# Kernel tuning notes

Measured on AMD Instinct MI355X. Metric: run time of the kernel, lower is better.

The kernel has to match this reference:

```python
import jax, jax.numpy as jnp
import numpy as np

N = 100_000
E = 1_000_000
D = 64
NORM_FACTOR = 100.0
LN_EPS = 1e-5


def setup_inputs() -> dict:
    key = jax.random.key(0)
    ks = jax.random.split(key, 8)
    h = jax.random.normal(ks[0], (N, D), dtype=jnp.float32)
    distances = jax.random.uniform(ks[1], (E, 1), dtype=jnp.float32)
    edges = jax.random.randint(ks[2], (2, E), 0, N, dtype=jnp.int64)
    node_mask = jnp.ones((N, 1), dtype=jnp.float32)
    edge_mask = jnp.ones((E, 1), dtype=jnp.float32)
    s = 1.0 / np.sqrt(D)
    W_lin = jax.random.normal(ks[3], (D, D), dtype=jnp.float32) * s
    b_lin = jnp.zeros((D,), dtype=jnp.float32)
    att_W1 = jax.random.normal(ks[4], (D, 2 * D + 1), dtype=jnp.float32) * (1.0 / np.sqrt(2 * D + 1))
    att_b1 = jnp.zeros((D,), dtype=jnp.float32)
    att_W2 = jax.random.normal(ks[5], (1, D), dtype=jnp.float32) * s
    att_b2 = jnp.zeros((1,), dtype=jnp.float32)
    ln_g = jnp.ones((D,), dtype=jnp.float32)
    ln_b = jnp.zeros((D,), dtype=jnp.float32)
    return {"h": h, "distances": distances, "edges": edges, "node_mask": node_mask,
            "edge_mask": edge_mask, "W_lin": W_lin, "b_lin": b_lin,
            "att_W1": att_W1, "att_b1": att_b1, "att_W2": att_W2, "att_b2": att_b2,
            "ln_g": ln_g, "ln_b": ln_b}


def reference(h, distances, edges, node_mask, edge_mask, W_lin, b_lin,
              att_W1, att_b1, att_W2, att_b2, ln_g, ln_b):
    # Linear projection: [N, D]
    x = h @ W_lin.T + b_lin
    row, col = edges[0], edges[1]
    x_row = x[row]          # [E, D]
    x_col = x[col]          # [E, D]
    # DenseAtt: MLP(concat(x_row, x_col, dist)) -> sigmoid -> * edge_mask
    cat = jnp.concatenate([x_row, x_col, distances], axis=1)  # [E, 2D+1]
    hdn = jax.nn.silu(cat @ att_W1.T + att_b1)                # [E, D]
    att = jax.nn.sigmoid(hdn @ att_W2.T + att_b2) * edge_mask # [E, 1]
    # Attention-weighted scatter-sum aggregation into row segments
    agg = x_col * att
    out = jax.ops.segment_sum(agg, row, num_segments=x.shape[0]) / NORM_FACTOR
    out = out + x           # residual
    # LayerNorm + activation
    mu = jnp.mean(out, axis=-1, keepdims=True)
    var = jnp.mean(jnp.square(out - mu), axis=-1, keepdims=True)
    y = (out - mu) * jax.lax.rsqrt(var + LN_EPS) * ln_g + ln_b
    return jax.nn.silu(y)
```

## Files before the change

### kernel.cpp

```cpp
#include <hip/hip_runtime.h>
#include <hip/hip_bf16.h>

#define N_NODES 100000
#define N_EDGES 1000000
#define DIM 64
#define NORM_INV 0.01f
#define LN_EPS 1e-5f
#define N_TILES 6250
#define PROJ_BLOCKS 1563
#define N_BUCKETS 782
#define HISTB 489
#define L2E 1.4426950408889634f
#define LN2 0.6931471805599453f
#define CAP 2560
#define RPT 5

typedef __attribute__((ext_vector_type(8))) short short8;
typedef __attribute__((ext_vector_type(4))) float f32x4;

__device__ __forceinline__ unsigned short f2bf(float f) {
    union { float f; unsigned u; } x; x.f = f;
    unsigned r = x.u + 0x7FFFu + ((x.u >> 16) & 1u);
    return (unsigned short)(r >> 16);
}
__device__ __forceinline__ float bf2f(unsigned short s) {
    union { unsigned u; float f; } x; x.u = ((unsigned)s) << 16; return x.f;
}

__global__ __launch_bounds__(256) void prep_frags(
    const float* __restrict__ W, const float* __restrict__ att_W1,
    const float* __restrict__ att_b1, const float* __restrict__ att_W2,
    short8* __restrict__ whi, short8* __restrict__ wlo,
    short8* __restrict__ wa, short8* __restrict__ wb,
    float4* __restrict__ tab) {
    const int l = threadIdx.x & 63;
    const int nt = threadIdx.x >> 6;
    const int c = l & 15, q = l >> 4;
    const int n = nt * 16 + c;
#pragma unroll
    for (int ks = 0; ks < 2; ++ks) {
        const int k0 = ks * 32 + q * 8;
        short8 hi8, lo8, a8, b8;
#pragma unroll
        for (int jj = 0; jj < 8; ++jj) {
            float w = W[n * 64 + k0 + jj];
            unsigned short hh = f2bf(w);
            hi8[jj] = (short)hh;
            lo8[jj] = (short)f2bf(w - bf2f(hh));
            a8[jj] = (short)f2bf(att_W1[n * 129 + k0 + jj]);
            b8[jj] = (short)f2bf(att_W1[n * 129 + 64 + k0 + jj]);
        }
        const int idx = (nt * 2 + ks) * 64 + l;
        whi[idx] = hi8; wlo[idx] = lo8; wa[idx] = a8; wb[idx] = b8;
    }
    if (threadIdx.x < 64) {
        const int f = threadIdx.x;
        tab[f] = make_float4(att_W2[f] * LN2, att_W1[f * 129 + 128] * L2E,
                             att_b1[f] * L2E, 0.f);
    }
}

__global__ __launch_bounds__(256) void proj_hist(
    const float* __restrict__ h, const float* __restrict__ bl,
    const short8* __restrict__ whi, const short8* __restrict__ wlo,
    const short8* __restrict__ wa, const short8* __restrict__ wb,
    const int* __restrict__ edges, int* __restrict__ bucketCnt,
    unsigned short* __restrict__ xv, unsigned short* __restrict__ u_bf) {
    if (blockIdx.x >= PROJ_BLOCKS) {
        __shared__ int lh[N_BUCKETS];
        const int tid = threadIdx.x;
        for (int i = tid; i < N_BUCKETS; i += 256) lh[i] = 0;
        __syncthreads();
        const int e0 = (blockIdx.x - PROJ_BLOCKS) * 2048;
#pragma unroll
        for (int i = 0; i < 8; ++i) {
            const int e = e0 + tid * 8 + i;
            if (e < N_EDGES) atomicAdd(&lh[edges[e] >> 7], 1);
        }
        __syncthreads();
        for (int b = tid; b < N_BUCKETS; b += 256)
            if (lh[b]) atomicAdd(&bucketCnt[b], lh[b]);
        return;
    }
    __shared__ __align__(16) unsigned short lds[4][16 * 72];
    const int lane = threadIdx.x & 63;
    const int wv = threadIdx.x >> 6;
    const int c = lane & 15, q = lane >> 4;
    const int tile = blockIdx.x * 4 + wv;
    if (tile >= N_TILES) return;
    const int n0 = tile * 16;

    short8 Whi[4][2], Wlo[4][2], Wa[4][2], Wb[4][2];
    float bias[4];
#pragma unroll
    for (int nt = 0; nt < 4; ++nt) {
        bias[nt] = bl[nt * 16 + c];
#pragma unroll
        for (int ks = 0; ks < 2; ++ks) {
            const int idx = (nt * 2 + ks) * 64 + lane;
            Whi[nt][ks] = whi[idx]; Wlo[nt][ks] = wlo[idx];
            Wa[nt][ks] = wa[idx];   Wb[nt][ks] = wb[idx];
        }
    }

    short8 Ahi[2], Alo[2];
#pragma unroll
    for (int ks = 0; ks < 2; ++ks) {
        const float* hp = h + (size_t)(n0 + c) * 64 + ks * 32 + q * 8;
        f32x4 p0 = *(const f32x4*)hp;
        f32x4 p1 = *(const f32x4*)(hp + 4);
        short8 hi8, lo8;
#pragma unroll
        for (int jj = 0; jj < 4; ++jj) {
            unsigned short hh = f2bf(p0[jj]);
            hi8[jj] = (short)hh; lo8[jj] = (short)f2bf(p0[jj] - bf2f(hh));
            unsigned short h2 = f2bf(p1[jj]);
            hi8[4 + jj] = (short)h2; lo8[4 + jj] = (short)f2bf(p1[jj] - bf2f(h2));
        }
        Ahi[ks] = hi8; Alo[ks] = lo8;
    }

    f32x4 xacc[4] = {{0,0,0,0},{0,0,0,0},{0,0,0,0},{0,0,0,0}};
#pragma unroll
    for (int ks = 0; ks < 2; ++ks)
#pragma unroll
        for (int nt = 0; nt < 4; ++nt) {
            xacc[nt] = __builtin_amdgcn_mfma_f32_16x16x32_bf16(Ahi[ks], Whi[nt][ks], xacc[nt], 0, 0, 0);
            xacc[nt] = __builtin_amdgcn_mfma_f32_16x16x32_bf16(Ahi[ks], Wlo[nt][ks], xacc[nt], 0, 0, 0);
            xacc[nt] = __builtin_amdgcn_mfma_f32_16x16x32_bf16(Alo[ks], Whi[nt][ks], xacc[nt], 0, 0, 0);
        }

    unsigned short* lw = lds[wv];
#pragma unroll
    for (int r = 0; r < 4; ++r) {
        const int node = n0 + q * 4 + r;
        unsigned short xb[4];
#pragma unroll
        for (int nt = 0; nt < 4; ++nt) {
            unsigned short v16 = f2bf(xacc[nt][r] + bias[nt]);
            xb[nt] = v16;
            lw[(q * 4 + r) * 72 + nt * 16 + c] = v16;
        }
        uint2 pk;
        pk.x = (unsigned)xb[0] | ((unsigned)xb[1] << 16);
        pk.y = (unsigned)xb[2] | ((unsigned)xb[3] << 16);
        *(uint2*)(xv + (size_t)node * 128 + c * 8) = pk;
    }

    short8 Ax[2];
#pragma unroll
    for (int ks = 0; ks < 2; ++ks)
        Ax[ks] = *(const short8*)&lw[c * 72 + ks * 32 + q * 8];

    f32x4 uacc[4] = {{0,0,0,0},{0,0,0,0},{0,0,0,0},{0,0,0,0}};
    f32x4 vacc[4] = {{0,0,0,0},{0,0,0,0},{0,0,0,0},{0,0,0,0}};
#pragma unroll
    for (int ks = 0; ks < 2; ++ks)
#pragma unroll
        for (int nt = 0; nt < 4; ++nt) {
            uacc[nt] = __builtin_amdgcn_mfma_f32_16x16x32_bf16(Ax[ks], Wa[nt][ks], uacc[nt], 0, 0, 0);
            vacc[nt] = __builtin_amdgcn_mfma_f32_16x16x32_bf16(Ax[ks], Wb[nt][ks], vacc[nt], 0, 0, 0);
        }
#pragma unroll
    for (int r = 0; r < 4; ++r) {
        const int node = n0 + q * 4 + r;
        uint2 pu;
        pu.x = (unsigned)f2bf(uacc[0][r] * L2E) | ((unsigned)f2bf(uacc[1][r] * L2E) << 16);
        pu.y = (unsigned)f2bf(uacc[2][r] * L2E) | ((unsigned)f2bf(uacc[3][r] * L2E) << 16);
        *(uint2*)(u_bf + (size_t)node * 64 + c * 4) = pu;
        uint2 pk;
        pk.x = (unsigned)f2bf(vacc[0][r] * L2E) | ((unsigned)f2bf(vacc[1][r] * L2E) << 16);
        pk.y = (unsigned)f2bf(vacc[2][r] * L2E) | ((unsigned)f2bf(vacc[3][r] * L2E) << 16);
        *(uint2*)(xv + (size_t)node * 128 + c * 8 + 4) = pk;
    }
}

__global__ __launch_bounds__(1024) void scanA(
    const int* __restrict__ bucketCnt, int* __restrict__ baseA,
    int* __restrict__ cursA) {
    __shared__ int wsum[16];
    const int t = threadIdx.x, lane = t & 63, w = t >> 6;
    const int v = (t < N_BUCKETS) ? bucketCnt[t] : 0;
    int sc = v;
#pragma unroll
    for (int off = 1; off < 64; off <<= 1) {
        int u = __shfl_up(sc, off);
        if (lane >= off) sc += u;
    }
    if (lane == 63) wsum[w] = sc;
    __syncthreads();
    if (w == 0) {
        int x = (lane < 16) ? wsum[lane] : 0;
#pragma unroll
        for (int off = 1; off < 16; off <<= 1) {
            int u = __shfl_up(x, off);
            if (lane >= off) x += u;
        }
        if (lane < 16) wsum[lane] = x;
    }
    __syncthreads();
    const int excl = sc - v + ((w > 0) ? wsum[w - 1] : 0);
    if (t < N_BUCKETS) { baseA[t] = excl; cursA[t] = excl; }
    if (t == N_BUCKETS - 1) baseA[N_BUCKETS] = excl + v;
}

__global__ __launch_bounds__(256) void scatterA(
    const int* __restrict__ edges, const float* __restrict__ dist,
    const float* __restrict__ emask, int* __restrict__ cursA,
    uint2* __restrict__ srec, unsigned char* __restrict__ lrowS) {
    __shared__ int lh[N_BUCKETS];
    __shared__ int lb[N_BUCKETS];
    const int tid = threadIdx.x;
    for (int i = tid; i < N_BUCKETS; i += 256) lh[i] = 0;
    __syncthreads();

    const int e0 = blockIdx.x * 2048 + tid * 8;
    int row[8], col[8];
    unsigned de[8];
#pragma unroll
    for (int i = 0; i < 8; ++i) {
        const int e = e0 + i;
        if (e < N_EDGES) {
            row[i] = edges[e];
            col[i] = edges[N_EDGES + e];
            de[i] = (unsigned)f2bf(dist[e]) | ((unsigned)f2bf(emask[e] * NORM_INV) << 16);
            atomicAdd(&lh[row[i] >> 7], 1);
        } else {
            row[i] = -1;
        }
    }
    __syncthreads();
    for (int b = tid; b < N_BUCKETS; b += 256) {
        const int c = lh[b];
        lb[b] = c ? atomicAdd(&cursA[b], c) : 0;
    }
    __syncthreads();
    for (int i = tid; i < N_BUCKETS; i += 256) lh[i] = 0;
    __syncthreads();
#pragma unroll
    for (int i = 0; i < 8; ++i) {
        if (row[i] >= 0) {
            const int bk = row[i] >> 7;
            const int rk = atomicAdd(&lh[bk], 1);
            const int pos = lb[bk] + rk;
            uint2 rc; rc.x = (unsigned)col[i]; rc.y = de[i];
            srec[pos] = rc;
            lrowS[pos] = (unsigned char)(row[i] & 127);
        }
    }
}

__global__ __launch_bounds__(512, 4) void agg_fused(
    const int* __restrict__ baseA, const unsigned char* __restrict__ lrowS,
    const uint2* __restrict__ srec,
    const unsigned short* __restrict__ xv, const unsigned short* __restrict__ u_bf,
    const float4* __restrict__ tab, const float* __restrict__ att_b2,
    const float* __restrict__ ln_g, const float* __restrict__ ln_b,
    float* __restrict__ out) {
    __shared__ __align__(16) uint2 lrecs[CAP + 16];
    __shared__ int hist[128];
    __shared__ int rst[129];
    __shared__ int cur[128];
    __shared__ int wtot;

    const int b = blockIdx.x;
    const int tid = threadIdx.x;
    const int lane = tid & 63;
    const int wv = tid >> 6;
    const int s0g = baseA[b];
    const int cnt = baseA[b + 1] - s0g;

    if (tid < 128) hist[tid] = 0;
    __syncthreads();

    uint2 rec0, rec1, rec2, rec3, rec4;
    int lr0 = -1, lr1 = -1, lr2 = -1, lr3 = -1, lr4 = -1;
    {
        int idx = tid;
        if (idx < cnt) { rec0 = srec[s0g + idx]; lr0 = lrowS[s0g + idx]; atomicAdd(&hist[lr0], 1); }
        idx += 512;
        if (idx < cnt) { rec1 = srec[s0g + idx]; lr1 = lrowS[s0g + idx]; atomicAdd(&hist[lr1], 1); }
        idx += 512;
        if (idx < cnt) { rec2 = srec[s0g + idx]; lr2 = lrowS[s0g + idx]; atomicAdd(&hist[lr2], 1); }
        idx += 512;
        if (idx < cnt) { rec3 = srec[s0g + idx]; lr3 = lrowS[s0g + idx]; atomicAdd(&hist[lr3], 1); }
        idx += 512;
        if (idx < cnt) { rec4 = srec[s0g + idx]; lr4 = lrowS[s0g + idx]; atomicAdd(&hist[lr4], 1); }
    }
    __syncthreads();

    int c = 0, p = 0, sc = 0;
    if (tid < 128) {
        c = hist[tid];
        p = (c + 3) & ~3;
        sc = p;
#pragma unroll
        for (int off = 1; off < 64; off <<= 1) {
            int u = __shfl_up(sc, off);
            if (lane >= off) sc += u;
        }
        if (tid == 63) wtot = sc;
    }
    __syncthreads();
    if (tid < 128) {
        if (tid >= 64) sc += wtot;
        const int excl = sc - p;
        rst[tid] = excl;
        cur[tid] = excl;
        uint2 z; z.x = 0; z.y = 0;
        for (int i = c; i < p; ++i) lrecs[excl + i] = z;
        if (tid == 127) {
            rst[128] = excl + p;
            for (int i = 0; i < 16; ++i) lrecs[excl + p + i] = z;
        }
    }
    __syncthreads();

    if (lr0 >= 0) lrecs[atomicAdd(&cur[lr0], 1)] = rec0;
    if (lr1 >= 0) lrecs[atomicAdd(&cur[lr1], 1)] = rec1;
    if (lr2 >= 0) lrecs[atomicAdd(&cur[lr2], 1)] = rec2;
    if (lr3 >= 0) lrecs[atomicAdd(&cur[lr3], 1)] = rec3;
    if (lr4 >= 0) lrecs[atomicAdd(&cur[lr4], 1)] = rec4;
    __syncthreads();

    const int j = lane & 15;
    const int sl = lane >> 4;
    const float4 t0 = tab[j], t1 = tab[j + 16], t2 = tab[j + 32], t3 = tab[j + 48];
    const float b2L = att_b2[0] * L2E;
    const float gg = ln_g[lane], bb = ln_b[lane];
    const unsigned* xvu = (const unsigned*)xv;

#pragma unroll 1
    for (int k = 0; k < 16; ++k) {
        const int lrw = wv + 8 * k;
        const int r = b * 128 + lrw;
        if (r >= N_NODES) break;

        const uint2 uu = *(const uint2*)(u_bf + (size_t)r * 64 + j * 4);
        const float base0 = __uint_as_float(uu.x << 16) + t0.z;
        const float base1 = __uint_as_float(uu.x & 0xffff0000u) + t1.z;
        const float base2 = __uint_as_float(uu.y << 16) + t2.z;
        const float base3 = __uint_as_float(uu.y & 0xffff0000u) + t3.z;

        const int s0 = rst[lrw];
        const int e1 = rst[lrw + 1];

        float a0 = 0.f, a1 = 0.f, a2 = 0.f, a3 = 0.f;
        if (e1 > s0) {
            uint2 recA = lrecs[s0 + sl];
            uint4 xvA = *(const uint4*)(xvu + (size_t)recA.x * 64 + j * 4);
            for (int e = s0; e < e1; e += 4) {
                const uint2 recB = lrecs[e + 4 + sl];
                const uint4 xvB = *(const uint4*)(xvu + (size_t)recB.x * 64 + j * 4);

                const float dist = __uint_as_float(recA.y << 16);
                const float emN = __uint_as_float(recA.y & 0xffff0000u);
                const float x0 = __uint_as_float(xvA.x << 16);
                const float x1 = __uint_as_float(xvA.x & 0xffff0000u);
                const float x2 = __uint_as_float(xvA.y << 16);
                const float x3 = __uint_as_float(xvA.y & 0xffff0000u);
                const float v0 = __uint_as_float(xvA.z << 16);
                const float v1 = __uint_as_float(xvA.z & 0xffff0000u);
                const float v2 = __uint_as_float(xvA.w << 16);
                const float v3 = __uint_as_float(xvA.w & 0xffff0000u);
                float pv = 0.f, pre, sg;
                pre = fmaf(dist, t0.y, base0) + v0;
                sg = __builtin_amdgcn_rcpf(1.f + __builtin_amdgcn_exp2f(-pre));
                pv = fmaf(pre * sg, t0.x, pv);
                pre = fmaf(dist, t1.y, base1) + v1;
                sg = __builtin_amdgcn_rcpf(1.f + __builtin_amdgcn_exp2f(-pre));
                pv = fmaf(pre * sg, t1.x, pv);
                pre = fmaf(dist, t2.y, base2) + v2;
                sg = __builtin_amdgcn_rcpf(1.f + __builtin_amdgcn_exp2f(-pre));
                pv = fmaf(pre * sg, t2.x, pv);
                pre = fmaf(dist, t3.y, base3) + v3;
                sg = __builtin_amdgcn_rcpf(1.f + __builtin_amdgcn_exp2f(-pre));
                pv = fmaf(pre * sg, t3.x, pv);
                pv += __shfl_xor(pv, 1); pv += __shfl_xor(pv, 2);
                pv += __shfl_xor(pv, 4); pv += __shfl_xor(pv, 8);
                const float sp = fmaf(pv, L2E, b2L);
                const float att =
                    emN * __builtin_amdgcn_rcpf(1.f + __builtin_amdgcn_exp2f(-sp));
                a0 = fmaf(att, x0, a0); a1 = fmaf(att, x1, a1);
                a2 = fmaf(att, x2, a2); a3 = fmaf(att, x3, a3);
                recA = recB; xvA = xvB;
            }
        }
        a0 += __shfl_xor(a0, 16); a0 += __shfl_xor(a0, 32);
        a1 += __shfl_xor(a1, 16); a1 += __shfl_xor(a1, 32);
        a2 += __shfl_xor(a2, 16); a2 += __shfl_xor(a2, 32);
        a3 += __shfl_xor(a3, 16); a3 += __shfl_xor(a3, 32);

        const uint2 xr = *(const uint2*)(xvu + (size_t)r * 64 + j * 4);
        const float o0 = __uint_as_float(xr.x << 16) + a0;
        const float o1 = __uint_as_float(xr.x & 0xffff0000u) + a1;
        const float o2 = __uint_as_float(xr.y << 16) + a2;
        const float o3 = __uint_as_float(xr.y & 0xffff0000u) + a3;

        float ssum = o0 + o1 + o2 + o3;
        ssum += __shfl_xor(ssum, 1); ssum += __shfl_xor(ssum, 2);
        ssum += __shfl_xor(ssum, 4); ssum += __shfl_xor(ssum, 8);
        const float mu = ssum * (1.f / 64.f);
        const float d0 = o0 - mu, d1 = o1 - mu, d2 = o2 - mu, d3 = o3 - mu;
        float vs = d0 * d0 + d1 * d1 + d2 * d2 + d3 * d3;
        vs += __shfl_xor(vs, 1); vs += __shfl_xor(vs, 2);
        vs += __shfl_xor(vs, 4); vs += __shfl_xor(vs, 8);
        const float rstd = rsqrtf(vs * (1.f / 64.f) + LN_EPS);

        const float dk = (sl == 0) ? d0 : (sl == 1) ? d1 : (sl == 2) ? d2 : d3;
        const float y = fmaf(dk * rstd, gg, bb);
        out[(size_t)r * 64 + lane] =
            y * __builtin_amdgcn_rcpf(1.f + __builtin_amdgcn_exp2f(-y * L2E));
    }
}

extern "C" void kernel_launch(void* const* d_in, const int* in_sizes, int n_in,
                              void* d_out, int out_size, void* d_ws, size_t ws_size,
                              hipStream_t stream) {
    const float* h      = (const float*)d_in[0];
    const float* dist   = (const float*)d_in[1];
    const int*   edges  = (const int*)d_in[2];
    const float* emask  = (const float*)d_in[4];
    const float* W_lin  = (const float*)d_in[5];
    const float* b_lin  = (const float*)d_in[6];
    const float* att_W1 = (const float*)d_in[7];
    const float* att_b1 = (const float*)d_in[8];
    const float* att_W2 = (const float*)d_in[9];
    const float* att_b2 = (const float*)d_in[10];
    const float* ln_g   = (const float*)d_in[11];
    const float* ln_b   = (const float*)d_in[12];
    float* out = (float*)d_out;

    char* ws = (char*)d_ws;
    unsigned short* xv   = (unsigned short*)ws;
    unsigned short* u_bf = (unsigned short*)(ws + 25600000);
    uint2* srec          = (uint2*)(ws + 38400000);
    unsigned char* lrowS = (unsigned char*)(ws + 46400000);
    int* bucketCnt       = (int*)(ws + 47400000);
    int* baseA           = (int*)(ws + 47403200);
    int* cursA           = (int*)(ws + 47406400);
    float4* tab          = (float4*)(ws + 47409600);
    short8* whi          = (short8*)(ws + 47410624);
    short8* wlo          = (short8*)(ws + 47418816);
    short8* wa           = (short8*)(ws + 47427008);
    short8* wb           = (short8*)(ws + 47435200);

    hipMemsetAsync(bucketCnt, 0, N_BUCKETS * sizeof(int), stream);
    prep_frags<<<1, 256, 0, stream>>>(W_lin, att_W1, att_b1, att_W2,
                                      whi, wlo, wa, wb, tab);
    proj_hist<<<PROJ_BLOCKS + HISTB, 256, 0, stream>>>(
        h, b_lin, whi, wlo, wa, wb, edges, bucketCnt, xv, u_bf);
    scanA<<<1, 1024, 0, stream>>>(bucketCnt, baseA, cursA);
    scatterA<<<HISTB, 256, 0, stream>>>(edges, dist, emask, cursA, srec, lrowS);
    agg_fused<<<N_BUCKETS, 512, 0, stream>>>(baseA, lrowS, srec, xv, u_bf,
                                             tab, att_b2, ln_g, ln_b, out);
}
```

Before: 237.6 us.

## Sort edges locally in shared memory before scatter and pack row into record

The scatter kernel now processes 4096 edges per block with vectorized loads, does a local counting sort in shared memory by bucket, then writes each bucket's records out as contiguous runs instead of scattered single writes. The 7-bit local row index is packed into the top byte of the column field, which removes the separate lrowS byte array from both the scatter and the aggregation kernels. This targets uncoalesced global writes and extra memory traffic. The cost is heavier shared-memory use per block, fewer blocks, and column indices limited to 24 bits.

```diff
diff --git a/kernel.cpp b/kernel.cpp
--- a/kernel.cpp
+++ b/kernel.cpp
@@ -9,11 +9,13 @@
 #define N_TILES 6250
 #define PROJ_BLOCKS 1563
 #define N_BUCKETS 782
+#define NB_PAD 800
 #define HISTB 489
+#define SC_EDGES 4096
+#define SC_BLOCKS 245
 #define L2E 1.4426950408889634f
 #define LN2 0.6931471805599453f
 #define CAP 2560
-#define RPT 5
 
 typedef __attribute__((ext_vector_type(8))) short short8;
 typedef __attribute__((ext_vector_type(4))) float f32x4;
@@ -204,55 +206,118 @@
     if (t == N_BUCKETS - 1) baseA[N_BUCKETS] = excl + v;
 }
 
-__global__ __launch_bounds__(256) void scatterA(
+__global__ __launch_bounds__(256) void scatterB(
     const int* __restrict__ edges, const float* __restrict__ dist,
     const float* __restrict__ emask, int* __restrict__ cursA,
-    uint2* __restrict__ srec, unsigned char* __restrict__ lrowS) {
-    __shared__ int lh[N_BUCKETS];
-    __shared__ int lb[N_BUCKETS];
+    uint2* __restrict__ srec) {
+    __shared__ int lh[NB_PAD];
+    __shared__ int lofs[NB_PAD];
+    __shared__ int lb[NB_PAD];
+    __shared__ __align__(16) uint2 lsort[SC_EDGES];
+    __shared__ unsigned short gb[SC_EDGES];
+    __shared__ int wsum[4];
+
     const int tid = threadIdx.x;
-    for (int i = tid; i < N_BUCKETS; i += 256) lh[i] = 0;
-    __syncthreads();
-
-    const int e0 = blockIdx.x * 2048 + tid * 8;
-    int row[8], col[8];
-    unsigned de[8];
-#pragma unroll
-    for (int i = 0; i < 8; ++i) {
-        const int e = e0 + i;
-        if (e < N_EDGES) {
-            row[i] = edges[e];
-            col[i] = edges[N_EDGES + e];
-            de[i] = (unsigned)f2bf(dist[e]) | ((unsigned)f2bf(emask[e] * NORM_INV) << 16);
-            atomicAdd(&lh[row[i] >> 7], 1);
+    const int lane = tid & 63;
+    const int w = tid >> 6;
+    for (int i = tid; i < NB_PAD; i += 256) lh[i] = 0;
+    __syncthreads();
+
+    const int eb = blockIdx.x * SC_EDGES;
+    const int total = min(SC_EDGES, N_EDGES - eb);
+
+    int rows[16], rank[16];
+    uint2 recs[16];
+    const int e0 = eb + tid * 16;
+#pragma unroll
+    for (int g = 0; g < 4; ++g) {
+        const int e = e0 + g * 4;
+        if (e + 4 <= N_EDGES) {
+            const int4 rr = *(const int4*)(edges + e);
+            const int4 cc = *(const int4*)(edges + N_EDGES + e);
+            const float4 dd = *(const float4*)(dist + e);
+            const float4 mm = *(const float4*)(emask + e);
+            rows[g*4+0] = rr.x; rows[g*4+1] = rr.y; rows[g*4+2] = rr.z; rows[g*4+3] = rr.w;
+            const int c4[4] = {cc.x, cc.y, cc.z, cc.w};
+            const float d4[4] = {dd.x, dd.y, dd.z, dd.w};
+            const float m4[4] = {mm.x, mm.y, mm.z, mm.w};
+#pragma unroll
+            for (int i = 0; i < 4; ++i) {
+                const int ii = g * 4 + i;
+                recs[ii].x = (unsigned)c4[i] | ((unsigned)(rows[ii] & 127) << 24);
+                recs[ii].y = (unsigned)f2bf(d4[i]) |
+                             ((unsigned)f2bf(m4[i] * NORM_INV) << 16);
+                rank[ii] = atomicAdd(&lh[rows[ii] >> 7], 1);
+            }
         } else {
-            row[i] = -1;
-        }
-    }
-    __syncthreads();
-    for (int b = tid; b < N_BUCKETS; b += 256) {
-        const int c = lh[b];
-        lb[b] = c ? atomicAdd(&cursA[b], c) : 0;
-    }
-    __syncthreads();
-    for (int i = tid; i < N_BUCKETS; i += 256) lh[i] = 0;
-    __syncthreads();
-#pragma unroll
-    for (int i = 0; i < 8; ++i) {
-        if (row[i] >= 0) {
-            const int bk = row[i] >> 7;
-            const int rk = atomicAdd(&lh[bk], 1);
-            const int pos = lb[bk] + rk;
-            uint2 rc; rc.x = (unsigned)col[i]; rc.y = de[i];
-            srec[pos] = rc;
-            lrowS[pos] = (unsigned char)(row[i] & 127);
-        }
+#pragma unroll
+            for (int i = 0; i < 4; ++i) {
+                const int ii = g * 4 + i;
+                const int ee = e + i;
+                if (ee < N_EDGES) {
+                    rows[ii] = edges[ee];
+                    recs[ii].x = (unsigned)edges[N_EDGES + ee] |
+                                 ((unsigned)(rows[ii] & 127) << 24);
+                    recs[ii].y = (unsigned)f2bf(dist[ee]) |
+                                 ((unsigned)f2bf(emask[ee] * NORM_INV) << 16);
+                    rank[ii] = atomicAdd(&lh[rows[ii] >> 7], 1);
+                } else {
+                    rows[ii] = -1;
+                }
+            }
+        }
+    }
+    __syncthreads();
+
+    const int b0 = tid * 4;
+    int c0 = 0, c1 = 0, c2 = 0, c3 = 0;
+    if (b0 < NB_PAD) { c0 = lh[b0]; c1 = lh[b0+1]; c2 = lh[b0+2]; c3 = lh[b0+3]; }
+    const int S = c0 + c1 + c2 + c3;
+    int sc = S;
+#pragma unroll
+    for (int off = 1; off < 64; off <<= 1) {
+        int u = __shfl_up(sc, off);
+        if (lane >= off) sc += u;
+    }
+    if (lane == 63) wsum[w] = sc;
+    __syncthreads();
+    int wbase = 0;
+    if (w > 0) wbase = wsum[0];
+    if (w > 1) wbase += wsum[1];
+    if (w > 2) wbase += wsum[2];
+    int excl = sc - S + wbase;
+    if (b0 < N_BUCKETS) {
+        lofs[b0] = excl;
+        lofs[b0+1] = excl + c0;
+        lofs[b0+2] = excl + c0 + c1;
+        lofs[b0+3] = excl + c0 + c1 + c2;
+        if (c0) lb[b0]   = atomicAdd(&cursA[b0],   c0);
+        if (c1 && b0+1 < N_BUCKETS) lb[b0+1] = atomicAdd(&cursA[b0+1], c1);
+        if (c2 && b0+2 < N_BUCKETS) lb[b0+2] = atomicAdd(&cursA[b0+2], c2);
+        if (c3 && b0+3 < N_BUCKETS) lb[b0+3] = atomicAdd(&cursA[b0+3], c3);
+    }
+    __syncthreads();
+
+#pragma unroll
+    for (int i = 0; i < 16; ++i) {
+        if (rows[i] >= 0) {
+            const int bk = rows[i] >> 7;
+            const int pos = lofs[bk] + rank[i];
+            lsort[pos] = recs[i];
+            gb[pos] = (unsigned short)bk;
+        }
+    }
+    __syncthreads();
+
+    for (int s = tid; s < total; s += 256) {
+        const int bk = gb[s];
+        const uint2 rc = lsort[s];
+        srec[lb[bk] + (s - lofs[bk])] = rc;
     }
 }
 
 __global__ __launch_bounds__(512, 4) void agg_fused(
-    const int* __restrict__ baseA, const unsigned char* __restrict__ lrowS,
-    const uint2* __restrict__ srec,
+    const int* __restrict__ baseA, const uint2* __restrict__ srec,
     const unsigned short* __restrict__ xv, const unsigned short* __restrict__ u_bf,
     const float4* __restrict__ tab, const float* __restrict__ att_b2,
     const float* __restrict__ ln_g, const float* __restrict__ ln_b,
@@ -277,15 +342,15 @@
     int lr0 = -1, lr1 = -1, lr2 = -1, lr3 = -1, lr4 = -1;
     {
         int idx = tid;
-        if (idx < cnt) { rec0 = srec[s0g + idx]; lr0 = lrowS[s0g + idx]; atomicAdd(&hist[lr0], 1); }
+        if (idx < cnt) { rec0 = srec[s0g + idx]; lr0 = (int)(rec0.x >> 24); rec0.x &= 0x00FFFFFFu; atomicAdd(&hist[lr0], 1); }
         idx += 512;
-        if (idx < cnt) { rec1 = srec[s0g + idx]; lr1 = lrowS[s0g + idx]; atomicAdd(&hist[lr1], 1); }
+        if (idx < cnt) { rec1 = srec[s0g + idx]; lr1 = (int)(rec1.x >> 24); rec1.x &= 0x00FFFFFFu; atomicAdd(&hist[lr1], 1); }
         idx += 512;
-        if (idx < cnt) { rec2 = srec[s0g + idx]; lr2 = lrowS[s0g + idx]; atomicAdd(&hist[lr2], 1); }
+        if (idx < cnt) { rec2 = srec[s0g + idx]; lr2 = (int)(rec2.x >> 24); rec2.x &= 0x00FFFFFFu; atomicAdd(&hist[lr2], 1); }
         idx += 512;
-        if (idx < cnt) { rec3 = srec[s0g + idx]; lr3 = lrowS[s0g + idx]; atomicAdd(&hist[lr3], 1); }
+        if (idx < cnt) { rec3 = srec[s0g + idx]; lr3 = (int)(rec3.x >> 24); rec3.x &= 0x00FFFFFFu; atomicAdd(&hist[lr3], 1); }
         idx += 512;
-        if (idx < cnt) { rec4 = srec[s0g + idx]; lr4 = lrowS[s0g + idx]; atomicAdd(&hist[lr4], 1); }
+        if (idx < cnt) { rec4 = srec[s0g + idx]; lr4 = (int)(rec4.x >> 24); rec4.x &= 0x00FFFFFFu; atomicAdd(&hist[lr4], 1); }
     }
     __syncthreads();
 
@@ -435,15 +500,14 @@
     unsigned short* xv   = (unsigned short*)ws;
     unsigned short* u_bf = (unsigned short*)(ws + 25600000);
     uint2* srec          = (uint2*)(ws + 38400000);
-    unsigned char* lrowS = (unsigned char*)(ws + 46400000);
-    int* bucketCnt       = (int*)(ws + 47400000);
-    int* baseA           = (int*)(ws + 47403200);
-    int* cursA           = (int*)(ws + 47406400);
-    float4* tab          = (float4*)(ws + 47409600);
-    short8* whi          = (short8*)(ws + 47410624);
-    short8* wlo          = (short8*)(ws + 47418816);
-    short8* wa           = (short8*)(ws + 47427008);
-    short8* wb           = (short8*)(ws + 47435200);
+    int* bucketCnt       = (int*)(ws + 46400000);
+    int* baseA           = (int*)(ws + 46403200);
+    int* cursA           = (int*)(ws + 46406400);
+    float4* tab          = (float4*)(ws + 46409600);
+    short8* whi          = (short8*)(ws + 46410624);
+    short8* wlo          = (short8*)(ws + 46418816);
+    short8* wa           = (short8*)(ws + 46427008);
+    short8* wb           = (short8*)(ws + 46435200);
 
     hipMemsetAsync(bucketCnt, 0, N_BUCKETS * sizeof(int), stream);
     prep_frags<<<1, 256, 0, stream>>>(W_lin, att_W1, att_b1, att_W2,
@@ -451,7 +515,7 @@
     proj_hist<<<PROJ_BLOCKS + HISTB, 256, 0, stream>>>(
         h, b_lin, whi, wlo, wa, wb, edges, bucketCnt, xv, u_bf);
     scanA<<<1, 1024, 0, stream>>>(bucketCnt, baseA, cursA);
-    scatterA<<<HISTB, 256, 0, stream>>>(edges, dist, emask, cursA, srec, lrowS);
-    agg_fused<<<N_BUCKETS, 512, 0, stream>>>(baseA, lrowS, srec, xv, u_bf,
+    scatterB<<<SC_BLOCKS, 256, 0, stream>>>(edges, dist, emask, cursA, srec);
+    agg_fused<<<N_BUCKETS, 512, 0, stream>>>(baseA, srec, xv, u_bf,
                                              tab, att_b2, ln_g, ln_b, out);
 }
```

After: 232.9 us. -2.0%, faster.
